# Kernel tuning notes

Measured on AMD Instinct MI355X. Metric: run time of the kernel, lower is better.

The kernel has to match this reference:

```python
import jax, jax.numpy as jnp
import numpy as np

STATE_DIM = 128
ACT_DIM = 32
ENC_K = 10   # encoder_spine_dim
DEC_K = 10   # decoder_dim
H0, H1 = 2048, 2048
BATCH = 16384
MAX_ACTION = 1.0
STD0 = 0.3872983346207417  # sqrt(0.15)


def setup_inputs() -> dict:
    key = jax.random.key(0)
    ks = jax.random.split(key, 10)
    state = jax.random.normal(ks[0], (BATCH, STATE_DIM), dtype=jnp.float32)
    # encoder params: mean linspace over mean_range, std constant
    mean_enc = jnp.broadcast_to(jnp.linspace(-3.0, 3.0, ENC_K, dtype=jnp.float32),
                                (1, STATE_DIM, ENC_K))
    std_enc = jnp.full((1, STATE_DIM, ENC_K), STD0, dtype=jnp.float32)
    def lin(k, fan_in, fan_out):
        bound = 1.0 / np.sqrt(fan_in)
        k1, k2 = jax.random.split(k)
        W = jax.random.uniform(k1, (fan_out, fan_in), jnp.float32, -bound, bound)
        b = jax.random.uniform(k2, (fan_out,), jnp.float32, -bound, bound)
        return W, b
    W1, b1 = lin(ks[1], STATE_DIM * ENC_K, H0)
    W2, b2 = lin(ks[2], H0, H1)
    W3, b3 = lin(ks[3], H1, ACT_DIM * DEC_K)
    # grouped conv1d: weight [act_dim, 1, dec_k], bias [act_dim]
    bound = 1.0 / np.sqrt(DEC_K)
    Wd = jax.random.uniform(ks[4], (ACT_DIM, 1, DEC_K), jnp.float32, -bound, bound)
    bd = jax.random.uniform(ks[5], (ACT_DIM,), jnp.float32, -bound, bound)
    return {"state": state, "mean_enc": mean_enc, "std_enc": std_enc,
            "W1": W1, "b1": b1, "W2": W2, "b2": b2, "W3": W3, "b3": b3,
            "Wd": Wd, "bd": bd}


def reference(state, mean_enc, std_enc, W1, b1, W2, b2, W3, b3, Wd, bd):
    # Population-coding encoder: sigmoid((obs - mean)/std), flattened
    spine = jax.nn.sigmoid((state[:, :, None] - mean_enc) / std_enc)  # [B, D, K]
    spine = spine.reshape(state.shape[0], -1)                         # [B, D*K]
    a = jax.nn.relu(spine @ W1.T + b1)
    a = jax.nn.relu(a @ W2.T + b2)
    a = a @ W3.T + b3                                                 # [B, A*Kd]
    d = a.reshape(-1, ACT_DIM, DEC_K)                                 # [B, A, Kd]
    # grouped Conv1d with kernel == length => per-channel dot product
    raw = jnp.einsum('bak,ak->ba', d, Wd[:, 0, :]) + bd               # [B, A]
    return MAX_ACTION * jnp.tanh(raw)
```

## Files before the change

kernel.cpp:

```cpp
#include <hip/hip_runtime.h>
#include <hip/hip_bf16.h>
#include <stdint.h>

#define BATCH   16384
#define SDIM    128
#define ENCK    10
#define ADIM    32
#define DECK    10
#define HID     2048
#define KSPINE  1280

typedef __bf16 bf16x8 __attribute__((ext_vector_type(8)));
typedef float  f32x4  __attribute__((ext_vector_type(4)));

typedef __attribute__((address_space(1))) const void kGlobalVoid;
typedef __attribute__((address_space(3))) void       kLdsVoid;

__device__ __forceinline__ unsigned short f2b(float f) {
  union { float f; unsigned u; } v; v.f = f;
  unsigned r = v.u + 0x7fffu + ((v.u >> 16) & 1u);
  return (unsigned short)(r >> 16);
}

__device__ __forceinline__ int permrow(int pr) {
  int q = pr & 63;
  return (pr & ~63) | (((q & 15) << 2) | (q >> 4));
}

#define ENC_BLKS  40960
#define W1_BLKS   5120
#define W2_BLKS   8192
#define WEFF_BLKS 256

__global__ __launch_bounds__(256) void prep_kernel(
    const float* __restrict__ state, const float* __restrict__ mean,
    const float* __restrict__ stdv,
    const float* __restrict__ W1, const float* __restrict__ W2,
    const float* __restrict__ W3, const float* __restrict__ Wd,
    const float* __restrict__ b3, const float* __restrict__ bd,
    unsigned* __restrict__ spine, unsigned* __restrict__ W1b,
    unsigned* __restrict__ W2b, unsigned short* __restrict__ Weff,
    float* __restrict__ beff) {
  int b = blockIdx.x, t = threadIdx.x;
  if (b < ENC_BLKS) {
    int idx = b * 256 + t;
    int idx1 = (int)(((long long)idx * 0x66666667LL) >> 33);
    int kk = idx - idx1 * 5;
    int d  = idx1 & (SDIM - 1);
    float x = state[idx1];
    int mi = d * ENCK + kk * 2;
    float m0 = mean[mi], m1 = mean[mi + 1];
    float s0 = stdv[mi], s1 = stdv[mi + 1];
    float v0 = 1.f / (1.f + __expf((m0 - x) / s0));
    float v1 = 1.f / (1.f + __expf((m1 - x) / s1));
    spine[idx] = (unsigned)f2b(v0) | ((unsigned)f2b(v1) << 16);
  } else if (b < ENC_BLKS + W1_BLKS) {
    int i = (b - ENC_BLKS) * 256 + t;
    int row = i / 640, c2 = i - row * 640;
    float2 v = reinterpret_cast<const float2*>(W1)[permrow(row) * 640 + c2];
    W1b[i] = (unsigned)f2b(v.x) | ((unsigned)f2b(v.y) << 16);
  } else if (b < ENC_BLKS + W1_BLKS + W2_BLKS) {
    int i = (b - ENC_BLKS - W1_BLKS) * 256 + t;
    int row = i >> 10, c2 = i & 1023;
    float2 v = reinterpret_cast<const float2*>(W2)[permrow(row) * 1024 + c2];
    W2b[i] = (unsigned)f2b(v.x) | ((unsigned)f2b(v.y) << 16);
  } else if (b < ENC_BLKS + W1_BLKS + W2_BLKS + WEFF_BLKS) {
    int idx = (b - ENC_BLKS - W1_BLKS - W2_BLKS) * 256 + t;
    int a = idx >> 11, j = idx & 2047;
    float s = 0.f;
#pragma unroll
    for (int k = 0; k < DECK; ++k)
      s += Wd[a * DECK + k] * W3[(size_t)(a * DECK + k) * HID + j];
    Weff[idx] = f2b(s);
  } else {
    if (t < ADIM) {
      float s = bd[t];
#pragma unroll
      for (int k = 0; k < DECK; ++k) s += Wd[t * DECK + k] * b3[t * DECK + k];
      beff[t] = s;
    }
  }
}

#define A0B 0
#define B0B 32768
#define A1B 65536
#define B1B 98304

#define FENCE asm volatile("" ::: "memory")
#define SB0 __builtin_amdgcn_sched_barrier(0)
#define BAR __builtin_amdgcn_s_barrier()
#define LGKM0 do { asm volatile("s_waitcnt lgkmcnt(0)" ::: "memory"); SB0; } while (0)

#define STAGE(BASEPTR, R0A, R0B, LDS0, LDS1, KT)                                             \
  __builtin_amdgcn_global_load_lds((kGlobalVoid*)((BASEPTR) + (size_t)((R0A) + rs) * K + (KT) + ce), \
                                   (kLdsVoid*)(smem + (LDS0) + t * 16), 16, 0, 0);           \
  __builtin_amdgcn_global_load_lds((kGlobalVoid*)((BASEPTR) + (size_t)((R0B) + rs) * K + (KT) + ce), \
                                   (kLdsVoid*)(smem + (LDS1) + t * 16), 16, 0, 0);

#define DS_AF(DST, ABASE, MPN)                                                               \
  _Pragma("unroll")                                                                          \
  for (int j2 = 0; j2 < 2; ++j2) {                                                           \
    _Pragma("unroll")                                                                        \
    for (int ks = 0; ks < 2; ++ks) {                                                         \
      int rowl = wr * 128 + (MPN) * 32 + j2 * 16 + lr;                                       \
      DST[j2][ks] = *reinterpret_cast<const bf16x8*>(                                        \
          smem + (ABASE) + rowl * 128 + ((((ks) << 6) | (kh << 4)) ^ swz));                  \
    }                                                                                        \
  }

#define DS_B2(DST, NP, BBASE)                                                                \
  _Pragma("unroll")                                                                          \
  for (int ks = 0; ks < 2; ++ks) {                                                           \
    int rowl = wc * 64 + (NP) * 16 + lr;                                                     \
    DST[NP][ks] = *reinterpret_cast<const bf16x8*>(                                          \
        smem + (BBASE) + rowl * 128 + ((((ks) << 6) | (kh << 4)) ^ swz));                    \
  }

#define DS_BF(DST, BBASE)                                                                    \
  _Pragma("unroll")                                                                          \
  for (int n = 0; n < 4; ++n) {                                                              \
    _Pragma("unroll")                                                                        \
    for (int ks = 0; ks < 2; ++ks) {                                                         \
      int rowl = wc * 64 + n * 16 + lr;                                                      \
      DST[n][ks] = *reinterpret_cast<const bf16x8*>(                                         \
          smem + (BBASE) + rowl * 128 + ((((ks) << 6) | (kh << 4)) ^ swz));                  \
    }                                                                                        \
  }

#define MFMA16(MP, AF, BF)                                                                   \
  _Pragma("unroll")                                                                          \
  for (int j2 = 0; j2 < 2; ++j2)                                                             \
    _Pragma("unroll")                                                                        \
    for (int n = 0; n < 4; ++n)                                                              \
      _Pragma("unroll")                                                                      \
      for (int ks = 0; ks < 2; ++ks)                                                         \
        acc[(MP) * 2 + j2][n] = __builtin_amdgcn_mfma_f32_16x16x32_bf16(                     \
            AF[j2][ks], BF[n][ks], acc[(MP) * 2 + j2][n], 0, 0, 0);

#define SGB_PHASE                                                                            \
  __builtin_amdgcn_sched_group_barrier(0x8, 2, 0);                                           \
  __builtin_amdgcn_sched_group_barrier(0x100, 1, 0);                                         \
  __builtin_amdgcn_sched_group_barrier(0x8, 2, 0);                                           \
  __builtin_amdgcn_sched_group_barrier(0x100, 1, 0);                                         \
  __builtin_amdgcn_sched_group_barrier(0x20, 2, 0);                                          \
  __builtin_amdgcn_sched_group_barrier(0x8, 3, 0);                                           \
  __builtin_amdgcn_sched_group_barrier(0x100, 1, 0);                                         \
  __builtin_amdgcn_sched_group_barrier(0x8, 3, 0);                                           \
  __builtin_amdgcn_sched_group_barrier(0x100, 1, 0);                                         \
  __builtin_amdgcn_sched_group_barrier(0x8, 3, 0);                                           \
  __builtin_amdgcn_sched_group_barrier(0x100, 1, 0);                                         \
  __builtin_amdgcn_sched_group_barrier(0x8, 3, 0);                                           \
  __builtin_amdgcn_sched_group_barrier(0x100, 1, 0);

#define VM_NONE
#define VM2 asm volatile("s_waitcnt vmcnt(2)" ::: "memory"); SB0;
#define VM6 asm volatile("s_waitcnt vmcnt(6)" ::: "memory"); SB0;

#define PH(MP, AF_C, AF_N, BF_C, BF_N, NXT_A, NXT_MP, BBASE_N, VMW, STG)                     \
  do {                                                                                       \
    LGKM0;                                                                                   \
    VMW                                                                                      \
    __builtin_amdgcn_s_setprio(1);                                                           \
    MFMA16(MP, AF_C, BF_C);                                                                  \
    __builtin_amdgcn_s_setprio(0);                                                           \
    DS_AF(AF_N, NXT_A, NXT_MP);                                                              \
    DS_B2(BF_N, MP, BBASE_N);                                                                \
    STG;                                                                                     \
    SGB_PHASE;                                                                               \
    FENCE;                                                                                   \
    BAR;                                                                                     \
  } while (0)

#define GEMM_BODY                                                                            \
  __shared__ char smem[131072];                                                              \
  const int t    = threadIdx.x;                                                              \
  const int lane = t & 63;                                                                   \
  const int w    = t >> 6;                                                                   \
  const int wr   = w >> 2;                                                                   \
  const int wc   = w & 3;                                                                    \
  const int lr   = lane & 15;                                                                \
  const int kh   = lane >> 4;                                                                \
  const int swz  = (lr & 7) << 4;                                                            \
  const int rs   = t >> 3;                                                                   \
  const int ce   = ((t & 7) ^ (rs & 7)) << 3;                                                \
  const int bid = blockIdx.x;                                                                \
  const int xcd = bid & 7, idx = bid >> 3;                                                   \
  const int row0 = (xcd * 8 + (idx >> 3)) * 256;                                             \
  const int col0 = (idx & 7) * 256;                                                          \
  f32x4 acc[8][4];                                                                           \
  _Pragma("unroll")                                                                          \
  for (int m = 0; m < 8; ++m)                                                                \
    _Pragma("unroll")                                                                        \
    for (int n = 0; n < 4; ++n)                                                              \
      acc[m][n] = (f32x4){0.f, 0.f, 0.f, 0.f};                                               \
  bf16x8 afc[2][2], afn[2][2], bfA[4][2], bfB[4][2];                                         \
  STAGE(Bw, col0 + 0,   col0 + 64,  B0B + 0,     B0B + 8192,  0);                            \
  STAGE(Bw, col0 + 128, col0 + 192, B0B + 16384, B0B + 24576, 0);                            \
  STAGE(A,  row0 + 0,   row0 + 128, A0B + 0,     A0B + 16384, 0);                            \
  STAGE(A,  row0 + 64,  row0 + 192, A0B + 8192,  A0B + 24576, 0);                            \
  STAGE(Bw, col0 + 0,   col0 + 64,  B1B + 0,     B1B + 8192,  64);                           \
  STAGE(Bw, col0 + 128, col0 + 192, B1B + 16384, B1B + 24576, 64);                           \
  STAGE(A,  row0 + 0,   row0 + 128, A1B + 0,     A1B + 16384, 64);                           \
  asm volatile("s_waitcnt vmcnt(0)" ::: "memory");                                           \
  FENCE; BAR;                                                                                \
  DS_AF(afc, A0B, 0);                                                                        \
  DS_BF(bfA, B0B);                                                                           \
  for (int i = 0; i < NI; ++i) {                                                             \
    int kt0 = i << 7;                                                                        \
    int kt1 = kt0 + 64;                                                                      \
    int kt2 = kt0 + 128; if (kt2 >= K) kt2 -= K;                                             \
    int kt3 = kt0 + 192; if (kt3 >= K) kt3 -= K;                                             \
    PH(0, afc, afn, bfA, bfB, A0B, 1, B1B, VM2,                                              \
       STAGE(A,  row0 + 64,  row0 + 192, A1B + 8192,  A1B + 24576, kt1));                    \
    PH(1, afn, afc, bfA, bfB, A0B, 2, B1B, VM_NONE,                                          \
       STAGE(Bw, col0 + 0,   col0 + 64,  B0B + 0,     B0B + 8192,  kt2));                    \
    PH(2, afc, afn, bfA, bfB, A0B, 3, B1B, VM_NONE,                                          \
       STAGE(Bw, col0 + 128, col0 + 192, B0B + 16384, B0B + 24576, kt2));                    \
    PH(3, afn, afc, bfA, bfB, A1B, 0, B1B, VM6,                                              \
       STAGE(A,  row0 + 0,   row0 + 128, A0B + 0,     A0B + 16384, kt2));                    \
    PH(0, afc, afn, bfB, bfA, A1B, 1, B0B, VM2,                                              \
       STAGE(A,  row0 + 64,  row0 + 192, A0B + 8192,  A0B + 24576, kt2));                    \
    PH(1, afn, afc, bfB, bfA, A1B, 2, B0B, VM_NONE,                                          \
       STAGE(Bw, col0 + 0,   col0 + 64,  B1B + 0,     B1B + 8192,  kt3));                    \
    PH(2, afc, afn, bfB, bfA, A1B, 3, B0B, VM_NONE,                                          \
       STAGE(Bw, col0 + 128, col0 + 192, B1B + 16384, B1B + 24576, kt3));                    \
    PH(3, afn, afc, bfB, bfA, A0B, 0, B0B, VM6,                                              \
       STAGE(A,  row0 + 0,   row0 + 128, A1B + 0,     A1B + 16384, kt3));                    \
  }

__global__ __launch_bounds__(512, 2) void gemm_h1(
    const unsigned short* __restrict__ A, const unsigned short* __restrict__ Bw,
    const float* __restrict__ bias, unsigned short* __restrict__ Cout,
    int K, int NI) {
  GEMM_BODY

#pragma unroll
  for (int m = 0; m < 8; ++m) {
    int gr0 = row0 + wr * 128 + m * 16 + kh * 4;
    int cb  = col0 + wc * 64 + lr * 4;
    float bv0 = bias[cb], bv1 = bias[cb + 1], bv2 = bias[cb + 2], bv3 = bias[cb + 3];
#pragma unroll
    for (int v = 0; v < 4; ++v) {
      unsigned lo = (unsigned)f2b(fmaxf(acc[m][0][v] + bv0, 0.f)) |
                    ((unsigned)f2b(fmaxf(acc[m][1][v] + bv1, 0.f)) << 16);
      unsigned hi = (unsigned)f2b(fmaxf(acc[m][2][v] + bv2, 0.f)) |
                    ((unsigned)f2b(fmaxf(acc[m][3][v] + bv3, 0.f)) << 16);
      *reinterpret_cast<uint2*>(&Cout[(size_t)(gr0 + v) * 2048 + cb]) = make_uint2(lo, hi);
    }
  }
}

__global__ __launch_bounds__(512, 2) void gemm_dec(
    const unsigned short* __restrict__ A, const unsigned short* __restrict__ Bw,
    const float* __restrict__ bias, const unsigned short* __restrict__ Weff,
    float* __restrict__ out_part) {
  const int K = HID, NI = HID / 128;
  GEMM_BODY

  asm volatile("s_waitcnt vmcnt(0)" ::: "memory");
  LGKM0;
  FENCE; BAR;

#pragma unroll
  for (int m = 0; m < 8; ++m) {
    int r0  = wr * 128 + m * 16 + kh * 4;
    int cbl = wc * 64 + lr * 4;
    float bv0 = bias[col0 + cbl], bv1 = bias[col0 + cbl + 1];
    float bv2 = bias[col0 + cbl + 2], bv3 = bias[col0 + cbl + 3];
#pragma unroll
    for (int v = 0; v < 4; ++v) {
      int r = r0 + v;
      unsigned lo = (unsigned)f2b(fmaxf(acc[m][0][v] + bv0, 0.f)) |
                    ((unsigned)f2b(fmaxf(acc[m][1][v] + bv1, 0.f)) << 16);
      unsigned hi = (unsigned)f2b(fmaxf(acc[m][2][v] + bv2, 0.f)) |
                    ((unsigned)f2b(fmaxf(acc[m][3][v] + bv3, 0.f)) << 16);
      int byte = r * 512 + ((cbl * 2) ^ ((r & 7) << 4));
      *reinterpret_cast<uint2*>(smem + byte) = make_uint2(lo, hi);
    }
  }
  FENCE; BAR;

  f32x4 acc2[2][2];
#pragma unroll
  for (int mf = 0; mf < 2; ++mf)
#pragma unroll
    for (int nf = 0; nf < 2; ++nf) acc2[mf][nf] = (f32x4){0.f, 0.f, 0.f, 0.f};

#pragma unroll
  for (int kt = 0; kt < 256; kt += 32) {
    bf16x8 aF[2], bF[2];
#pragma unroll
    for (int mf = 0; mf < 2; ++mf) {
      int r = w * 32 + mf * 16 + lr;
      aF[mf] = *reinterpret_cast<const bf16x8*>(
          smem + r * 512 + (((kt + kh * 8) * 2) ^ ((r & 7) << 4)));
    }
#pragma unroll
    for (int nf = 0; nf < 2; ++nf)
      bF[nf] = *reinterpret_cast<const bf16x8*>(
          Weff + (size_t)(nf * 16 + lr) * HID + col0 + kt + kh * 8);
#pragma unroll
    for (int mf = 0; mf < 2; ++mf)
#pragma unroll
      for (int nf = 0; nf < 2; ++nf)
        acc2[mf][nf] = __builtin_amdgcn_mfma_f32_16x16x32_bf16(aF[mf], bF[nf], acc2[mf][nf], 0, 0, 0);
  }

  const int nb = idx & 7;
  float* op = out_part + (size_t)nb * BATCH * ADIM;
#pragma unroll
  for (int mf = 0; mf < 2; ++mf)
#pragma unroll
    for (int nf = 0; nf < 2; ++nf)
#pragma unroll
      for (int v = 0; v < 4; ++v) {
        int r = w * 32 + mf * 16 + kh * 4 + v;
        int a = nf * 16 + lr;
        op[(size_t)(row0 + r) * ADIM + a] = acc2[mf][nf][v];
      }
}

__global__ __launch_bounds__(256) void reduce_tanh(
    const float* __restrict__ part, const float* __restrict__ beff,
    float* __restrict__ out) {
  int i = blockIdx.x * 256 + threadIdx.x;
  float s = beff[i & 31];
#pragma unroll
  for (int nb = 0; nb < 8; ++nb) s += part[(size_t)nb * BATCH * ADIM + i];
  out[i] = tanhf(s);
}

extern "C" void kernel_launch(void* const* d_in, const int* in_sizes, int n_in,
                              void* d_out, int out_size, void* d_ws, size_t ws_size,
                              hipStream_t stream) {
  const float* state    = (const float*)d_in[0];
  const float* mean_enc = (const float*)d_in[1];
  const float* std_enc  = (const float*)d_in[2];
  const float* W1 = (const float*)d_in[3];
  const float* b1 = (const float*)d_in[4];
  const float* W2 = (const float*)d_in[5];
  const float* b2 = (const float*)d_in[6];
  const float* W3 = (const float*)d_in[7];
  const float* b3 = (const float*)d_in[8];
  const float* Wd = (const float*)d_in[9];
  const float* bd = (const float*)d_in[10];

  char* ws = (char*)d_ws;
  unsigned*       W1b   = (unsigned*)(ws + 0);
  unsigned*       W2b   = (unsigned*)(ws + 5242880);
  unsigned short* Weff  = (unsigned short*)(ws + 13631488);
  float*          beff  = (float*)(ws + 13762560);
  unsigned*       spine = (unsigned*)(ws + 13762688);
  unsigned short* h1    = (unsigned short*)(ws + 55705728);
  float*          part  = (float*)(ws + 122814592);

  prep_kernel<<<ENC_BLKS + W1_BLKS + W2_BLKS + WEFF_BLKS + 1, 256, 0, stream>>>(
      state, mean_enc, std_enc, W1, W2, W3, Wd, b3, bd,
      spine, W1b, W2b, Weff, beff);

  gemm_h1<<<512, 512, 0, stream>>>((const unsigned short*)spine, (const unsigned short*)W1b,
                                   b1, h1, KSPINE, KSPINE / 128);
  gemm_dec<<<512, 512, 0, stream>>>(h1, (const unsigned short*)W2b, b2, Weff, part);
  reduce_tanh<<<(BATCH * ADIM) / 256, 256, 0, stream>>>(part, beff, (float*)d_out);
}
```

Measured before the change: 233.2 us.

## Fuse split-N reduction and tanh into gemm_dec via last-block atomic counter

Removes the separate reduce_tanh kernel. Each gemm_dec block now fences its partial outputs and bumps an atomic counter for its row band, and the eighth block to arrive sums the eight partials, adds the bias and writes tanh. The intent is to save one kernel launch and to read the partials while they are likely still in cache. In exchange it adds a hipMemsetAsync on every call, threadfence costs, and a serialized tail of reduction work in the last block of each band.

After: 374.3 us. 1.61x slower.

```diff
diff --git a/kernel.cpp b/kernel.cpp
--- a/kernel.cpp
+++ b/kernel.cpp
@@ -254,7 +254,8 @@
 __global__ __launch_bounds__(512, 2) void gemm_dec(
     const unsigned short* __restrict__ A, const unsigned short* __restrict__ Bw,
     const float* __restrict__ bias, const unsigned short* __restrict__ Weff,
-    float* __restrict__ out_part) {
+    float* __restrict__ out_part, unsigned* __restrict__ cnt,
+    const float* __restrict__ beff, float* __restrict__ out) {
   const int K = HID, NI = HID / 128;
   GEMM_BODY
 
@@ -319,16 +320,28 @@
         int a = nf * 16 + lr;
         op[(size_t)(row0 + r) * ADIM + a] = acc2[mf][nf][v];
       }
-}
-
-__global__ __launch_bounds__(256) void reduce_tanh(
-    const float* __restrict__ part, const float* __restrict__ beff,
-    float* __restrict__ out) {
-  int i = blockIdx.x * 256 + threadIdx.x;
-  float s = beff[i & 31];
-#pragma unroll
-  for (int nb = 0; nb < 8; ++nb) s += part[(size_t)nb * BATCH * ADIM + i];
-  out[i] = tanhf(s);
+
+  __threadfence();
+  const int mband = xcd * 8 + (idx >> 3);
+  volatile unsigned* flag = reinterpret_cast<volatile unsigned*>(smem);
+  if (t == 0) {
+    unsigned old = atomicAdd(&cnt[mband], 1u);
+    *flag = (old == 7u) ? 1u : 0u;
+  }
+  __syncthreads();
+  if (*flag) {
+    __threadfence();
+#pragma unroll
+    for (int kk = 0; kk < 16; ++kk) {
+      int i = kk * 512 + t;
+      int r = i >> 5, a = i & 31;
+      float s = beff[a];
+#pragma unroll
+      for (int nbq = 0; nbq < 8; ++nbq)
+        s += out_part[((size_t)nbq * BATCH + row0 + r) * ADIM + a];
+      out[(size_t)(row0 + r) * ADIM + a] = tanhf(s);
+    }
+  }
 }
 
 extern "C" void kernel_launch(void* const* d_in, const int* in_sizes, int n_in,
@@ -351,9 +364,12 @@
   unsigned*       W2b   = (unsigned*)(ws + 5242880);
   unsigned short* Weff  = (unsigned short*)(ws + 13631488);
   float*          beff  = (float*)(ws + 13762560);
-  unsigned*       spine = (unsigned*)(ws + 13762688);
-  unsigned short* h1    = (unsigned short*)(ws + 55705728);
-  float*          part  = (float*)(ws + 122814592);
+  unsigned*       cnt   = (unsigned*)(ws + 13762688);
+  unsigned*       spine = (unsigned*)(ws + 13762944);
+  unsigned short* h1    = (unsigned short*)(ws + 55705984);
+  float*          part  = (float*)(ws + 122814848);
+
+  hipMemsetAsync(cnt, 0, 256, stream);
 
   prep_kernel<<<ENC_BLKS + W1_BLKS + W2_BLKS + WEFF_BLKS + 1, 256, 0, stream>>>(
       state, mean_enc, std_enc, W1, W2, W3, Wd, b3, bd,
@@ -361,6 +377,6 @@
 
   gemm_h1<<<512, 512, 0, stream>>>((const unsigned short*)spine, (const unsigned short*)W1b,
                                    b1, h1, KSPINE, KSPINE / 128);
-  gemm_dec<<<512, 512, 0, stream>>>(h1, (const unsigned short*)W2b, b2, Weff, part);
-  reduce_tanh<<<(BATCH * ADIM) / 256, 256, 0, stream>>>(part, beff, (float*)d_out);
-}
+  gemm_dec<<<512, 512, 0, stream>>>(h1, (const unsigned short*)W2b, b2, Weff, part,
+                                    cnt, beff, (float*)d_out);
+}
```
